# Optimization experiments

Measured on AMD Instinct MI355X. Metric: run time of the kernel, lower is better.

## Reference

```python
import jax, jax.numpy as jnp
import numpy as np

VOCAB = 100000
NUM_SPARSE = 26
NUM_DENSE = 13
EMBED_DIM = 128
BOT_DIMS = (512, 256, 128)
TOP_DIMS = (1024, 1024, 512, 256, 1)
BATCH = 16384
TOP_IN = (NUM_SPARSE + 1) * (NUM_SPARSE + 2) // 2 + EMBED_DIM  # 378 + 128 = 506


def _linear_params(key, d_in, d_out):
    kw, kb = jax.random.split(key)
    w = jax.random.normal(kw, (d_in, d_out), jnp.float32) * np.sqrt(2.0 / (d_in + d_out))
    b = jax.random.normal(kb, (d_out,), jnp.float32) * np.sqrt(1.0 / d_out)
    return w, b


def setup_inputs() -> dict:
    key = jax.random.key(0)
    ks = jax.random.split(key, 16)
    inp = {}
    inp['dense'] = jax.random.normal(ks[0], (BATCH, NUM_DENSE), jnp.float32)
    inp['cat'] = jax.random.randint(ks[1], (BATCH, NUM_SPARSE), 0, VOCAB, jnp.int32)
    # embedding table: uniform(0,1) scaled by 1/sqrt(vocab) per table (uniform vocab here)
    inp['emb'] = jax.random.uniform(ks[2], (NUM_SPARSE * VOCAB, EMBED_DIM), jnp.float32) / np.sqrt(VOCAB)
    d_in = NUM_DENSE
    for i, d_out in enumerate(BOT_DIMS):
        w, b = _linear_params(ks[3 + i], d_in, d_out)
        inp[f'bw{i}'] = w
        inp[f'bb{i}'] = b
        d_in = d_out
    d_in = TOP_IN
    for i, d_out in enumerate(TOP_DIMS):
        w, b = _linear_params(ks[8 + i], d_in, d_out)
        inp[f'tw{i}'] = w
        inp[f'tb{i}'] = b
        d_in = d_out
    return inp


def _forward(dense, cat, emb, bot_ws, bot_bs, top_ws, top_bs):
    B = dense.shape[0]
    # bottom MLP (all layers ReLU)
    h = dense
    for w, b in zip(bot_ws, bot_bs):
        h = jax.nn.relu(h @ w + b)
    bot_out = h  # (B, EMBED_DIM)
    # embedding gather with per-table offsets
    offsets = (jnp.arange(NUM_SPARSE, dtype=jnp.int32) * VOCAB)[None, :]
    idx = (cat + offsets).reshape(-1)
    embed_feats = jnp.take(emb, idx, axis=0).reshape(B, NUM_SPARSE, EMBED_DIM)
    # stack dense + sparse features: (B, 27, 128)
    feats = jnp.concatenate([bot_out[:, None, :], embed_feats], axis=1)
    # dot interaction: bmm then upper-triangular (incl. diagonal) extraction
    xact = jnp.einsum('bfd,bgd->bfg', feats, feats)  # (B, 27, 27)
    iu, ju = jnp.triu_indices(NUM_SPARSE + 1)
    interact = xact[:, iu, ju]  # (B, 378), row-major triu order matches torch
    top_in = jnp.concatenate([bot_out, interact], axis=-1)  # (B, 506)
    # top MLP: ReLU on all but last layer
    h = top_in
    n = len(top_ws)
    for i, (w, b) in enumerate(zip(top_ws, top_bs)):
        h = h @ w + b
        if i < n - 1:
            h = jax.nn.relu(h)
    return h  # (B, 1)


def reference(dense, cat, emb, bw0, bb0, bw1, bb1, bw2, bb2,
              tw0, tb0, tw1, tb1, tw2, tb2, tw3, tb3, tw4, tb4):
    return _forward(dense, cat, emb,
                    (bw0, bw1, bw2), (bb0, bb1, bb2),
                    (tw0, tw1, tw2, tw3, tw4), (tb0, tb1, tb2, tb3, tb4))
```

## Files before the change

### kernel.cpp

```cpp
#include <hip/hip_runtime.h>
#include <hip/hip_bf16.h>

typedef __bf16 bf16;
typedef __bf16 bf16x8 __attribute__((ext_vector_type(8)));
typedef float  f32x4  __attribute__((ext_vector_type(4)));
typedef float  f32x16 __attribute__((ext_vector_type(16)));

#define BATCH   16384
#define VOCAB   100000
#define NSPARSE 26

#define GLOBAL_AS __attribute__((address_space(1)))
#define LDS_AS    __attribute__((address_space(3)))

__device__ __forceinline__ void async_copy16(const bf16* g, bf16* l) {
    __builtin_amdgcn_global_load_lds((const GLOBAL_AS void*)g, (LDS_AS void*)l, 16, 0, 0);
}

__global__ void transpose_w_kernel(const float* __restrict__ w, bf16* __restrict__ wt,
                                   int K, int N, int Kpad) {
    int i = blockIdx.x * 256 + threadIdx.x;
    if (i >= N * Kpad) return;
    int n = i / Kpad;
    int k = i - n * Kpad;
    wt[i] = (k < K) ? (bf16)w[(size_t)k * N + n] : (bf16)0.f;
}

__global__ __launch_bounds__(256) void bot0_kernel(const float* __restrict__ dense,
                                                   const float* __restrict__ w,
                                                   const float* __restrict__ b,
                                                   bf16* __restrict__ h0) {
    __shared__ float ws_[13 * 512];
    __shared__ float ds_[8 * 13];
    int t  = threadIdx.x;
    int r0 = blockIdx.x * 8;
    for (int i = t; i < 13 * 512; i += 256) ws_[i] = w[i];
    for (int i = t; i < 8 * 13;   i += 256) ds_[i] = dense[(size_t)r0 * 13 + i];
    __syncthreads();
    float acc[8][2];
    for (int r = 0; r < 8; r++) { acc[r][0] = 0.f; acc[r][1] = 0.f; }
    for (int k = 0; k < 13; k++) {
        float w0 = ws_[k * 512 + t];
        float w1 = ws_[k * 512 + t + 256];
        for (int r = 0; r < 8; r++) {
            float d = ds_[r * 13 + k];
            acc[r][0] += d * w0;
            acc[r][1] += d * w1;
        }
    }
    float b0 = b[t], b1 = b[t + 256];
    for (int r = 0; r < 8; r++) {
        h0[(size_t)(r0 + r) * 512 + t]       = (bf16)fmaxf(acc[r][0] + b0, 0.f);
        h0[(size_t)(r0 + r) * 512 + t + 256] = (bf16)fmaxf(acc[r][1] + b1, 0.f);
    }
}

__global__ __launch_bounds__(256) void gemm_kernel(const bf16* __restrict__ A,
                                                   const bf16* __restrict__ Wt,
                                                   const float* __restrict__ bias,
                                                   bf16* __restrict__ C,
                                                   int M, int N, int K, int do_relu) {
    __shared__ bf16 As[128 * 32];
    __shared__ bf16 Ws[128 * 32];
    const int t    = threadIdx.x;
    const int wave = t >> 6;
    const int lane = t & 63;
    const int m0   = blockIdx.x * 128;
    const int n0   = blockIdx.y * 128;
    const int wm   = (wave & 1) * 64;
    const int wn   = (wave >> 1) * 64;
    const int q    = lane >> 4;
    const int l16  = lane & 15;

    const int srow = t >> 2;
    const int scol = (t & 3) * 8;
    const bf16* ag = A  + (size_t)(m0 + srow) * K + scol;
    const bf16* wg = Wt + (size_t)(n0 + srow) * K + scol;
    const size_t rowK64 = (size_t)64 * K;
    bf16* lA0 = &As[srow * 32 + scol];
    bf16* lA1 = &As[(64 + srow) * 32 + scol];
    bf16* lW0 = &Ws[srow * 32 + scol];
    bf16* lW1 = &Ws[(64 + srow) * 32 + scol];

    f32x4 acc[4][4];
    for (int mi = 0; mi < 4; mi++)
        for (int ni = 0; ni < 4; ni++)
            for (int r = 0; r < 4; r++) acc[mi][ni][r] = 0.f;

    for (int bk = 0; bk < K; bk += 32) {
        async_copy16(ag + bk,          lA0);
        async_copy16(ag + bk + rowK64, lA1);
        async_copy16(wg + bk,          lW0);
        async_copy16(wg + bk + rowK64, lW1);
        __syncthreads();
        bf16x8 af[4], bfr[4];
        for (int i = 0; i < 4; i++)
            af[i]  = *(const bf16x8*)&As[(wm + i * 16 + l16) * 32 + q * 8];
        for (int i = 0; i < 4; i++)
            bfr[i] = *(const bf16x8*)&Ws[(wn + i * 16 + l16) * 32 + q * 8];
        for (int mi = 0; mi < 4; mi++)
            for (int ni = 0; ni < 4; ni++)
                acc[mi][ni] = __builtin_amdgcn_mfma_f32_16x16x32_bf16(
                    af[mi], bfr[ni], acc[mi][ni], 0, 0, 0);
        __syncthreads();
    }

    for (int ni = 0; ni < 4; ni++) {
        int gn = n0 + wn + ni * 16 + l16;
        float bv = bias[gn];
        for (int mi = 0; mi < 4; mi++) {
            int gm = m0 + wm + mi * 16 + q * 4;
            for (int r = 0; r < 4; r++) {
                float v = acc[mi][ni][r] + bv;
                if (do_relu) v = fmaxf(v, 0.f);
                C[(size_t)(gm + r) * N + gn] = (bf16)v;
            }
        }
    }
}

__global__ __launch_bounds__(256) void interact_kernel(const int* __restrict__ cat,
                                                       const float* __restrict__ emb,
                                                       const bf16* __restrict__ bot,
                                                       bf16* __restrict__ top_in) {
    int wave = threadIdx.x >> 6;
    int lane = threadIdx.x & 63;
    int s = blockIdx.x * 4 + wave;
    int m = lane & 31;
    int h = lane >> 5;

    const float* erow = nullptr;
    if (m >= 1 && m <= NSPARSE) {
        int idx = cat[(size_t)s * NSPARSE + (m - 1)] + (m - 1) * VOCAB;
        erow = emb + (size_t)idx * 128;
    }
    const bf16* botp = bot + (size_t)s * 128;

    f32x16 acc;
    for (int r = 0; r < 16; r++) acc[r] = 0.f;

    for (int ck = 0; ck < 8; ck++) {
        bf16x8 frag;
        if (m == 0) {
            frag = *(const bf16x8*)(botp + ck * 16 + h * 8);
        } else if (erow) {
            const float* rp = erow + ck * 16 + h * 8;
            for (int j = 0; j < 8; j++) frag[j] = (bf16)rp[j];
        } else {
            for (int j = 0; j < 8; j++) frag[j] = (bf16)0.f;
        }
        acc = __builtin_amdgcn_mfma_f32_32x32x16_bf16(frag, frag, acc, 0, 0, 0);
    }

    bf16* tp = top_in + (size_t)s * 512;
    ((unsigned int*)tp)[lane] = ((const unsigned int*)botp)[lane];
    if (lane < 3) ((unsigned int*)tp)[253 + lane] = 0u;
    for (int r = 0; r < 16; r++) {
        int row = (r & 3) + 8 * (r >> 2) + 4 * h;
        int col = m;
        if (row <= col && col <= NSPARSE) {
            int tpos = row * 27 - (row * (row - 1)) / 2 + (col - row);
            tp[128 + tpos] = (bf16)acc[r];
        }
    }
}

__global__ __launch_bounds__(256) void out_kernel(const bf16* __restrict__ h,
                                                  const float* __restrict__ w,
                                                  const float* __restrict__ b,
                                                  float* __restrict__ out) {
    int wave = threadIdx.x >> 6;
    int lane = threadIdx.x & 63;
    int s = blockIdx.x * 4 + wave;
    const bf16* hp = h + (size_t)s * 256;
    float sum = 0.f;
    for (int j = 0; j < 4; j++)
        sum += (float)hp[lane * 4 + j] * w[lane * 4 + j];
    for (int off = 32; off > 0; off >>= 1)
        sum += __shfl_down(sum, off, 64);
    if (lane == 0) out[s] = sum + b[0];
}

extern "C" void kernel_launch(void* const* d_in, const int* in_sizes, int n_in,
                              void* d_out, int out_size, void* d_ws, size_t ws_size,
                              hipStream_t stream) {
    const float* dense = (const float*)d_in[0];
    const int*   cat   = (const int*)d_in[1];
    const float* emb   = (const float*)d_in[2];
    const float* bw0   = (const float*)d_in[3];
    const float* bb0   = (const float*)d_in[4];
    const float* bw1   = (const float*)d_in[5];
    const float* bb1   = (const float*)d_in[6];
    const float* bw2   = (const float*)d_in[7];
    const float* bb2   = (const float*)d_in[8];
    const float* tw0   = (const float*)d_in[9];
    const float* tb0   = (const float*)d_in[10];
    const float* tw1   = (const float*)d_in[11];
    const float* tb1   = (const float*)d_in[12];
    const float* tw2   = (const float*)d_in[13];
    const float* tb2   = (const float*)d_in[14];
    const float* tw3   = (const float*)d_in[15];
    const float* tb3   = (const float*)d_in[16];
    const float* tw4   = (const float*)d_in[17];
    const float* tb4   = (const float*)d_in[18];
    float* out = (float*)d_out;

    char* ws = (char*)d_ws;
    bf16* bufA = (bf16*)ws;  ws += (size_t)BATCH * 1024 * sizeof(bf16);
    bf16* bufB = (bf16*)ws;  ws += (size_t)BATCH * 1024 * sizeof(bf16);
    bf16* wtb1 = (bf16*)ws;  ws += (size_t)256  * 512  * sizeof(bf16);
    bf16* wtb2 = (bf16*)ws;  ws += (size_t)128  * 256  * sizeof(bf16);
    bf16* wtt0 = (bf16*)ws;  ws += (size_t)1024 * 512  * sizeof(bf16);
    bf16* wtt1 = (bf16*)ws;  ws += (size_t)1024 * 1024 * sizeof(bf16);
    bf16* wtt2 = (bf16*)ws;  ws += (size_t)512  * 1024 * sizeof(bf16);
    bf16* wtt3 = (bf16*)ws;  ws += (size_t)256  * 512  * sizeof(bf16);

    transpose_w_kernel<<<(256 * 512 + 255) / 256, 256, 0, stream>>>(bw1, wtb1, 512, 256, 512);
    transpose_w_kernel<<<(128 * 256 + 255) / 256, 256, 0, stream>>>(bw2, wtb2, 256, 128, 256);
    transpose_w_kernel<<<(1024 * 512 + 255) / 256, 256, 0, stream>>>(tw0, wtt0, 506, 1024, 512);
    transpose_w_kernel<<<(1024 * 1024 + 255) / 256, 256, 0, stream>>>(tw1, wtt1, 1024, 1024, 1024);
    transpose_w_kernel<<<(512 * 1024 + 255) / 256, 256, 0, stream>>>(tw2, wtt2, 1024, 512, 1024);
    transpose_w_kernel<<<(256 * 512 + 255) / 256, 256, 0, stream>>>(tw3, wtt3, 512, 256, 512);

    bot0_kernel<<<BATCH / 8, 256, 0, stream>>>(dense, bw0, bb0, bufA);
    gemm_kernel<<<dim3(BATCH / 128, 2), 256, 0, stream>>>(bufA, wtb1, bb1, bufB,
                                                          BATCH, 256, 512, 1);
    gemm_kernel<<<dim3(BATCH / 128, 1), 256, 0, stream>>>(bufB, wtb2, bb2, bufA,
                                                          BATCH, 128, 256, 1);

    interact_kernel<<<BATCH / 4, 256, 0, stream>>>(cat, emb, bufA, bufB);

    gemm_kernel<<<dim3(BATCH / 128, 8), 256, 0, stream>>>(bufB, wtt0, tb0, bufA,
                                                          BATCH, 1024, 512, 1);
    gemm_kernel<<<dim3(BATCH / 128, 8), 256, 0, stream>>>(bufA, wtt1, tb1, bufB,
                                                          BATCH, 1024, 1024, 1);
    gemm_kernel<<<dim3(BATCH / 128, 4), 256, 0, stream>>>(bufB, wtt2, tb2, bufA,
                                                          BATCH, 512, 1024, 1);
    gemm_kernel<<<dim3(BATCH / 128, 2), 256, 0, stream>>>(bufA, wtt3, tb3, bufB,
                                                          BATCH, 256, 512, 1);
    out_kernel<<<BATCH / 4, 256, 0, stream>>>(bufB, tw4, tb4, out);
}
```

Measured before the change: 1.711 ms.

## Add 256x256 pipelined GEMM for large top layers, batch tiled weight transposes

Adds a 512-thread GEMM kernel with 256x256 tiles, double-buffered LDS filled by async global-to-LDS copies, XOR-swizzled LDS layout, phased MFMA groups with priority hints and a workgroup swizzle. It is used for the two 1024-wide top layers, raising data reuse per tile and overlapping loads with compute. The six weight-transpose launches are merged into one coalesced 32x32 LDS-tiled transpose kernel, and the embedding gather now uses float4 loads. Larger tiles mean fewer workgroups (256 per GEMM) and heavy register and LDS use, which can lower occupancy or leave the GPU underfilled.

```diff
diff --git a/kernel.cpp b/kernel.cpp
--- a/kernel.cpp
+++ b/kernel.cpp
@@ -17,13 +17,38 @@
     __builtin_amdgcn_global_load_lds((const GLOBAL_AS void*)g, (LDS_AS void*)l, 16, 0, 0);
 }
 
-__global__ void transpose_w_kernel(const float* __restrict__ w, bf16* __restrict__ wt,
-                                   int K, int N, int Kpad) {
-    int i = blockIdx.x * 256 + threadIdx.x;
-    if (i >= N * Kpad) return;
-    int n = i / Kpad;
-    int k = i - n * Kpad;
-    wt[i] = (k < K) ? (bf16)w[(size_t)k * N + n] : (bf16)0.f;
+__global__ __launch_bounds__(256) void transpose_all_kernel(
+        const float* __restrict__ bw1, const float* __restrict__ bw2,
+        const float* __restrict__ tw0, const float* __restrict__ tw1,
+        const float* __restrict__ tw2, const float* __restrict__ tw3,
+        bf16* __restrict__ wtb1, bf16* __restrict__ wtb2,
+        bf16* __restrict__ wtt0, bf16* __restrict__ wtt1,
+        bf16* __restrict__ wtt2, bf16* __restrict__ wtt3) {
+    __shared__ float ld[32][33];
+    int bid = blockIdx.x;
+    const float* src; bf16* dst; int K, N, Kpad, tid;
+    if (bid < 128)       { src = bw1; dst = wtb1; K = 512;  N = 256;  Kpad = 512;  tid = bid; }
+    else if (bid < 160)  { src = bw2; dst = wtb2; K = 256;  N = 128;  Kpad = 256;  tid = bid - 128; }
+    else if (bid < 672)  { src = tw0; dst = wtt0; K = 506;  N = 1024; Kpad = 512;  tid = bid - 160; }
+    else if (bid < 1696) { src = tw1; dst = wtt1; K = 1024; N = 1024; Kpad = 1024; tid = bid - 672; }
+    else if (bid < 2208) { src = tw2; dst = wtt2; K = 1024; N = 512;  Kpad = 1024; tid = bid - 1696; }
+    else                 { src = tw3; dst = wtt3; K = 512;  N = 256;  Kpad = 512;  tid = bid - 2208; }
+    int tilesK = Kpad >> 5;
+    int tk = tid % tilesK, tn = tid / tilesK;
+    int k0 = tk * 32, n0 = tn * 32;
+    int tx = threadIdx.x & 31, ty = threadIdx.x >> 5;
+    #pragma unroll
+    for (int p = 0; p < 4; ++p) {
+        int kr = p * 8 + ty;
+        int gk = k0 + kr;
+        ld[kr][tx] = (gk < K) ? src[(size_t)gk * N + n0 + tx] : 0.f;
+    }
+    __syncthreads();
+    #pragma unroll
+    for (int p = 0; p < 4; ++p) {
+        int nr = p * 8 + ty;
+        dst[(size_t)(n0 + nr) * Kpad + k0 + tx] = (bf16)ld[tx][nr];
+    }
 }
 
 __global__ __launch_bounds__(256) void bot0_kernel(const float* __restrict__ dense,
@@ -119,6 +144,191 @@
     }
 }
 
+__device__ __forceinline__ void stage_q(bf16* Ls, const bf16* G, int K, int qd,
+                                        int kt, int t) {
+    int r0   = qd * 64 + (t >> 3);
+    int blkS = t & 7;
+    int blk  = blkS ^ (r0 & 7);
+    async_copy16(G + (size_t)r0 * K + kt * 64 + blk * 8,
+                 Ls + r0 * 64 + blkS * 8);
+    int r1 = r0 + 128;
+    async_copy16(G + (size_t)r1 * K + kt * 64 + blk * 8,
+                 Ls + r1 * 64 + blkS * 8);
+}
+
+__global__ __launch_bounds__(512, 2) void gemm256_kernel(const bf16* __restrict__ A,
+                                                         const bf16* __restrict__ Wt,
+                                                         const float* __restrict__ bias,
+                                                         bf16* __restrict__ C,
+                                                         int M, int N, int K, int do_relu) {
+    __shared__ __align__(16) bf16 As[2][256 * 64];
+    __shared__ __align__(16) bf16 Bs[2][256 * 64];
+    const int t    = threadIdx.x;
+    const int lane = t & 63;
+    const int wv   = t >> 6;
+    const int wr   = wv >> 2;
+    const int wc   = wv & 3;
+    const int l16  = lane & 15;
+    const int qd4  = lane >> 4;
+
+    const int nmt = gridDim.x;
+    const int nwg = gridDim.x * gridDim.y;
+    int lin = blockIdx.x + nmt * blockIdx.y;
+    int swz = ((nwg & 7) == 0) ? ((lin & 7) * (nwg >> 3) + (lin >> 3)) : lin;
+    const int m0 = (swz % nmt) * 256;
+    const int n0 = (swz / nmt) * 256;
+
+    const bf16* Ag = A  + (size_t)m0 * K;
+    const bf16* Bg = Wt + (size_t)n0 * K;
+    const int NW = K >> 6;
+
+    f32x4 acc[8][4];
+    #pragma unroll
+    for (int mi = 0; mi < 8; mi++)
+        #pragma unroll
+        for (int ni = 0; ni < 4; ni++)
+            #pragma unroll
+            for (int r = 0; r < 4; r++) acc[mi][ni][r] = 0.f;
+
+    stage_q(&As[0][0], Ag, K, 0, 0, t);
+    stage_q(&As[0][0], Ag, K, 1, 0, t);
+    stage_q(&Bs[0][0], Bg, K, 0, 0, t);
+    stage_q(&Bs[0][0], Bg, K, 1, 0, t);
+    if (NW > 1) {
+        stage_q(&As[1][0], Ag, K, 0, 1, t);
+        stage_q(&Bs[1][0], Bg, K, 0, 1, t);
+        stage_q(&Bs[1][0], Bg, K, 1, 1, t);
+        asm volatile("s_waitcnt vmcnt(6)" ::: "memory");
+    } else {
+        asm volatile("s_waitcnt vmcnt(0)" ::: "memory");
+    }
+    __builtin_amdgcn_s_barrier();
+    __builtin_amdgcn_sched_barrier(0);
+
+    bf16x8 af[4][2], bq0[2][2], bq1[2][2];
+
+    for (int w = 0; w < NW; ++w) {
+        const int db = w & 1;
+        bf16* Ab = &As[db][0];
+        bf16* Bb = &Bs[db][0];
+        bf16* Ao = &As[db ^ 1][0];
+
+        #pragma unroll
+        for (int mi = 0; mi < 4; ++mi) {
+            int row = wr * 128 + mi * 16 + l16;
+            #pragma unroll
+            for (int kk = 0; kk < 2; ++kk)
+                af[mi][kk] = *(const bf16x8*)(Ab + row * 64 + (((kk * 4 + qd4) ^ (row & 7)) * 8));
+        }
+        #pragma unroll
+        for (int ni = 0; ni < 2; ++ni) {
+            int row = wc * 64 + ni * 16 + l16;
+            #pragma unroll
+            for (int kk = 0; kk < 2; ++kk)
+                bq0[ni][kk] = *(const bf16x8*)(Bb + row * 64 + (((kk * 4 + qd4) ^ (row & 7)) * 8));
+        }
+        if (w + 1 < NW) stage_q(Ao, Ag, K, 1, w + 1, t);
+        __builtin_amdgcn_s_barrier();
+        __builtin_amdgcn_sched_barrier(0);
+        __builtin_amdgcn_s_setprio(1);
+        #pragma unroll
+        for (int kk = 0; kk < 2; ++kk)
+            #pragma unroll
+            for (int mi = 0; mi < 4; ++mi)
+                #pragma unroll
+                for (int ni = 0; ni < 2; ++ni)
+                    acc[mi][ni] = __builtin_amdgcn_mfma_f32_16x16x32_bf16(
+                        af[mi][kk], bq0[ni][kk], acc[mi][ni], 0, 0, 0);
+        __builtin_amdgcn_s_setprio(0);
+        __builtin_amdgcn_sched_barrier(0);
+        __builtin_amdgcn_s_barrier();
+        __builtin_amdgcn_sched_barrier(0);
+
+        #pragma unroll
+        for (int ni = 0; ni < 2; ++ni) {
+            int row = wc * 64 + (ni + 2) * 16 + l16;
+            #pragma unroll
+            for (int kk = 0; kk < 2; ++kk)
+                bq1[ni][kk] = *(const bf16x8*)(Bb + row * 64 + (((kk * 4 + qd4) ^ (row & 7)) * 8));
+        }
+        if (w + 2 < NW) stage_q(Ab, Ag, K, 0, w + 2, t);
+        __builtin_amdgcn_s_barrier();
+        __builtin_amdgcn_sched_barrier(0);
+        __builtin_amdgcn_s_setprio(1);
+        #pragma unroll
+        for (int kk = 0; kk < 2; ++kk)
+            #pragma unroll
+            for (int mi = 0; mi < 4; ++mi)
+                #pragma unroll
+                for (int ni = 0; ni < 2; ++ni)
+                    acc[mi][ni + 2] = __builtin_amdgcn_mfma_f32_16x16x32_bf16(
+                        af[mi][kk], bq1[ni][kk], acc[mi][ni + 2], 0, 0, 0);
+        __builtin_amdgcn_s_setprio(0);
+        __builtin_amdgcn_sched_barrier(0);
+        __builtin_amdgcn_s_barrier();
+        __builtin_amdgcn_sched_barrier(0);
+
+        #pragma unroll
+        for (int mi = 0; mi < 4; ++mi) {
+            int row = wr * 128 + (mi + 4) * 16 + l16;
+            #pragma unroll
+            for (int kk = 0; kk < 2; ++kk)
+                af[mi][kk] = *(const bf16x8*)(Ab + row * 64 + (((kk * 4 + qd4) ^ (row & 7)) * 8));
+        }
+        if (w + 2 < NW) stage_q(Bb, Bg, K, 0, w + 2, t);
+        __builtin_amdgcn_s_barrier();
+        __builtin_amdgcn_sched_barrier(0);
+        __builtin_amdgcn_s_setprio(1);
+        #pragma unroll
+        for (int kk = 0; kk < 2; ++kk)
+            #pragma unroll
+            for (int mi = 0; mi < 4; ++mi)
+                #pragma unroll
+                for (int ni = 0; ni < 2; ++ni)
+                    acc[mi + 4][ni] = __builtin_amdgcn_mfma_f32_16x16x32_bf16(
+                        af[mi][kk], bq0[ni][kk], acc[mi + 4][ni], 0, 0, 0);
+        __builtin_amdgcn_s_setprio(0);
+        __builtin_amdgcn_sched_barrier(0);
+        __builtin_amdgcn_s_barrier();
+        __builtin_amdgcn_sched_barrier(0);
+
+        if (w + 2 < NW) stage_q(Bb, Bg, K, 1, w + 2, t);
+        __builtin_amdgcn_s_barrier();
+        __builtin_amdgcn_sched_barrier(0);
+        __builtin_amdgcn_s_setprio(1);
+        #pragma unroll
+        for (int kk = 0; kk < 2; ++kk)
+            #pragma unroll
+            for (int mi = 0; mi < 4; ++mi)
+                #pragma unroll
+                for (int ni = 0; ni < 2; ++ni)
+                    acc[mi + 4][ni + 2] = __builtin_amdgcn_mfma_f32_16x16x32_bf16(
+                        af[mi][kk], bq1[ni][kk], acc[mi + 4][ni + 2], 0, 0, 0);
+        __builtin_amdgcn_s_setprio(0);
+        __builtin_amdgcn_sched_barrier(0);
+        if (w + 2 < NW) asm volatile("s_waitcnt vmcnt(6)" ::: "memory");
+        else            asm volatile("s_waitcnt vmcnt(0)" ::: "memory");
+        __builtin_amdgcn_s_barrier();
+        __builtin_amdgcn_sched_barrier(0);
+    }
+
+    #pragma unroll
+    for (int ni = 0; ni < 4; ++ni) {
+        int gn = n0 + wc * 64 + ni * 16 + l16;
+        float bv = bias[gn];
+        #pragma unroll
+        for (int mi = 0; mi < 8; ++mi) {
+            int gm = m0 + wr * 128 + mi * 16 + qd4 * 4;
+            #pragma unroll
+            for (int r = 0; r < 4; ++r) {
+                float v = acc[mi][ni][r] + bv;
+                if (do_relu) v = fmaxf(v, 0.f);
+                C[(size_t)(gm + r) * N + gn] = (bf16)v;
+            }
+        }
+    }
+}
+
 __global__ __launch_bounds__(256) void interact_kernel(const int* __restrict__ cat,
                                                        const float* __restrict__ emb,
                                                        const bf16* __restrict__ bot,
@@ -144,8 +354,10 @@
         if (m == 0) {
             frag = *(const bf16x8*)(botp + ck * 16 + h * 8);
         } else if (erow) {
-            const float* rp = erow + ck * 16 + h * 8;
-            for (int j = 0; j < 8; j++) frag[j] = (bf16)rp[j];
+            const float4* rp = (const float4*)(erow + ck * 16 + h * 8);
+            float4 u = rp[0], v = rp[1];
+            frag[0] = (bf16)u.x; frag[1] = (bf16)u.y; frag[2] = (bf16)u.z; frag[3] = (bf16)u.w;
+            frag[4] = (bf16)v.x; frag[5] = (bf16)v.y; frag[6] = (bf16)v.z; frag[7] = (bf16)v.w;
         } else {
             for (int j = 0; j < 8; j++) frag[j] = (bf16)0.f;
         }
@@ -215,12 +427,8 @@
     bf16* wtt2 = (bf16*)ws;  ws += (size_t)512  * 1024 * sizeof(bf16);
     bf16* wtt3 = (bf16*)ws;  ws += (size_t)256  * 512  * sizeof(bf16);
 
-    transpose_w_kernel<<<(256 * 512 + 255) / 256, 256, 0, stream>>>(bw1, wtb1, 512, 256, 512);
-    transpose_w_kernel<<<(128 * 256 + 255) / 256, 256, 0, stream>>>(bw2, wtb2, 256, 128, 256);
-    transpose_w_kernel<<<(1024 * 512 + 255) / 256, 256, 0, stream>>>(tw0, wtt0, 506, 1024, 512);
-    transpose_w_kernel<<<(1024 * 1024 + 255) / 256, 256, 0, stream>>>(tw1, wtt1, 1024, 1024, 1024);
-    transpose_w_kernel<<<(512 * 1024 + 255) / 256, 256, 0, stream>>>(tw2, wtt2, 1024, 512, 1024);
-    transpose_w_kernel<<<(256 * 512 + 255) / 256, 256, 0, stream>>>(tw3, wtt3, 512, 256, 512);
+    transpose_all_kernel<<<2336, 256, 0, stream>>>(bw1, bw2, tw0, tw1, tw2, tw3,
+                                                   wtb1, wtb2, wtt0, wtt1, wtt2, wtt3);
 
     bot0_kernel<<<BATCH / 8, 256, 0, stream>>>(dense, bw0, bb0, bufA);
     gemm_kernel<<<dim3(BATCH / 128, 2), 256, 0, stream>>>(bufA, wtb1, bb1, bufB,
@@ -230,10 +438,10 @@
 
     interact_kernel<<<BATCH / 4, 256, 0, stream>>>(cat, emb, bufA, bufB);
 
-    gemm_kernel<<<dim3(BATCH / 128, 8), 256, 0, stream>>>(bufB, wtt0, tb0, bufA,
-                                                          BATCH, 1024, 512, 1);
-    gemm_kernel<<<dim3(BATCH / 128, 8), 256, 0, stream>>>(bufA, wtt1, tb1, bufB,
-                                                          BATCH, 1024, 1024, 1);
+    gemm256_kernel<<<dim3(BATCH / 256, 4), 512, 0, stream>>>(bufB, wtt0, tb0, bufA,
+                                                             BATCH, 1024, 512, 1);
+    gemm256_kernel<<<dim3(BATCH / 256, 4), 512, 0, stream>>>(bufA, wtt1, tb1, bufB,
+                                                             BATCH, 1024, 1024, 1);
     gemm_kernel<<<dim3(BATCH / 128, 4), 256, 0, stream>>>(bufB, wtt2, tb2, bufA,
                                                           BATCH, 512, 1024, 1);
     gemm_kernel<<<dim3(BATCH / 128, 2), 256, 0, stream>>>(bufA, wtt3, tb3, bufB,
```

New measurement: 1.662 ms. -2.9%, faster.
